# Kernel optimization log

Hardware: AMD Instinct MI355X
Metric: run time of the kernel (lower is better)

Reference implementation:

```python
import jax, jax.numpy as jnp
import numpy as np
import math

C = 256
K = 64
STAGE_NUM = 3
UNFOLD_SIZES = (1, 3, 5)


def _l2norm(t, axis):
    return t / (1e-6 + jnp.linalg.norm(t, axis=axis, keepdims=True))


def setup_inputs() -> dict:
    key = jax.random.key(0)
    k0, k1, k2 = jax.random.split(key, 3)
    b, h, w = 4, 64, 64
    x = jax.random.normal(k0, (b, C, h, w), dtype=jnp.float32)
    mu0 = jax.random.normal(k1, (1, C, K), dtype=jnp.float32) * math.sqrt(2.0 / K)
    mu0 = _l2norm(mu0, axis=1)  # matches buffer init: normal_(0, sqrt(2/k)) then l2norm over c
    w_scalar = jnp.array(1.0, dtype=jnp.float32)
    # convcat: Conv2d(3c, c, 1); init std = sqrt(2 / (1*1*out_channels)) = sqrt(2/c)
    w_cat = jax.random.normal(k2, (C, 3 * C), dtype=jnp.float32) * math.sqrt(2.0 / C)
    b_cat = jnp.zeros((C,), dtype=jnp.float32)
    return {"x": x, "mu0": mu0, "w": w_scalar, "w_cat": w_cat, "b_cat": b_cat}


def _mwi_forward(x, mu0, w, w_cat, b_cat):
    b, c, h, wd = x.shape
    k = mu0.shape[2]
    mu = jnp.broadcast_to(mu0, (b, c, k))
    feats = []
    for s in UNFOLD_SIZES:
        p = (s - 1) // 2
        xp = jnp.pad(x, ((0, 0), (0, 0), (p, p), (p, p)))
        # im2col: (b, c, s*s, h, w), kernel positions row-major -> matches torch F.unfold then view(b,c,-1)
        patches = jnp.stack([xp[:, :, i:i + h, j:j + wd] for i in range(s) for j in range(s)], axis=2)
        ux = patches.reshape(b, c, s * s * h * wd)  # (b, c, N)
        z = None
        for _ in range(STAGE_NUM):  # EM iterations (no_grad in original)
            z = jax.nn.softmax(jnp.einsum('bcn,bck->bnk', ux, mu), axis=2)  # E-step
            z_ = z / (1e-6 + z.sum(axis=1, keepdims=True))
            mu = _l2norm(jnp.einsum('bcn,bnk->bck', ux, z_), axis=1)  # M-step
        mu = jax.lax.stop_gradient(mu)
        z = jax.lax.stop_gradient(z)
        zf = jnp.einsum('bck,bnk->bcn', mu, z)  # reconstruction (b, c, N)
        zf = zf.reshape(b, c, s, s, h, wd)
        # col2im (F.fold): overlap-add of kernel positions
        out = jnp.zeros((b, c, h + 2 * p, wd + 2 * p), dtype=x.dtype)
        for i in range(s):
            for j in range(s):
                out = out.at[:, :, i:i + h, j:j + wd].add(zf[:, :, i, j])
        feats.append(out[:, :, p:p + h, p:p + wd])
    cat = jnp.concatenate(feats, axis=1)  # (b, 3c, h, w)
    u = jnp.einsum('bihw,oi->bohw', cat, w_cat) + b_cat[None, :, None, None]
    out = jax.nn.relu(u * w + x)
    return out, mu


def reference(x, mu0, w, w_cat, b_cat):
    return _mwi_forward(x, mu0, w, w_cat, b_cat)
```

## Files before the change

### kernel.cpp

```cpp
#include <hip/hip_runtime.h>

typedef float f32x4 __attribute__((ext_vector_type(4)));
typedef short bf16x8 __attribute__((ext_vector_type(8)));
typedef unsigned short u16;
typedef u16 u16x8 __attribute__((ext_vector_type(8)));
typedef unsigned int u32;

#define B 4
#define C 256
#define K 64
#define NN 4096
#define W3C 768
#define CP 264
#define SP 72

__device__ __forceinline__ u16 bf_hi(float f) {
    unsigned u = __float_as_uint(f);
    u += 0x7FFFu + ((u >> 16) & 1u);
    return (u16)(u >> 16);
}
__device__ __forceinline__ float bf_f(u16 s) { return __uint_as_float(((unsigned)s) << 16); }

__global__ void k_prep(const float* __restrict__ x, const float* __restrict__ mu0,
                       const float* __restrict__ w_cat,
                       u16* __restrict__ xch, u16* __restrict__ xcl,
                       u16* __restrict__ wch, u16* __restrict__ wcl,
                       u16* __restrict__ muth, u16* __restrict__ mutl) {
    int blk = blockIdx.x, tid = threadIdx.x;
    if (blk < 2048) {
        int i = blk * 256 + tid;
        const float4* s4 = (const float4*)(x + (size_t)i * 8);
        float4 a = s4[0], bq = s4[1];
        float v[8] = {a.x, a.y, a.z, a.w, bq.x, bq.y, bq.z, bq.w};
        u16x8 hv, lv;
        #pragma unroll
        for (int j = 0; j < 8; j++) { u16 hh = bf_hi(v[j]); hv[j] = hh; lv[j] = bf_hi(v[j] - bf_f(hh)); }
        *(u16x8*)(xch + (size_t)i * 8) = hv;
        *(u16x8*)(xcl + (size_t)i * 8) = lv;
    } else if (blk < 2144) {
        int i = (blk - 2048) * 256 + tid;
        const float4* s4 = (const float4*)(w_cat + (size_t)i * 8);
        float4 a = s4[0], bq = s4[1];
        float v[8] = {a.x, a.y, a.z, a.w, bq.x, bq.y, bq.z, bq.w};
        u16x8 hv, lv;
        #pragma unroll
        for (int j = 0; j < 8; j++) { u16 hh = bf_hi(v[j]); hv[j] = hh; lv[j] = bf_hi(v[j] - bf_f(hh)); }
        *(u16x8*)(wch + (size_t)i * 8) = hv;
        *(u16x8*)(wcl + (size_t)i * 8) = lv;
    } else {
        int g = (blk - 2144) * 256 + tid;
        int kq = (g >> 8) & 63, cq = g & 255;
        float v = mu0[cq * K + kq];
        u16 hh = bf_hi(v);
        muth[g] = hh;
        mutl[g] = bf_hi(v - bf_f(hh));
    }
}

__global__ void k_prept(const float* __restrict__ x, u16* __restrict__ th,
                        u16* __restrict__ tl) {
    __shared__ float tile[32][33];
    int b = blockIdx.z, c0 = blockIdx.y * 32, n0 = blockIdx.x * 32;
    int tx = threadIdx.x, ty = threadIdx.y;
    #pragma unroll
    for (int j = 0; j < 4; j++)
        tile[ty + j * 8][tx] = x[((size_t)(b * C + c0 + ty + j * 8)) * NN + n0 + tx];
    __syncthreads();
    #pragma unroll
    for (int j = 0; j < 4; j++) {
        int n = n0 + ty + j * 8;
        float v = tile[tx][ty + j * 8];
        u16 hh = bf_hi(v);
        size_t o = ((size_t)(b * NN + n)) * C + c0 + tx;
        th[o] = hh;
        tl[o] = bf_hi(v - bf_f(hh));
    }
}

__global__ __launch_bounds__(256) void k_em(
        const u16* __restrict__ xth, const u16* __restrict__ xtl,
        const u16* __restrict__ xch, const u16* __restrict__ xcl,
        const u16* __restrict__ muth, const u16* __restrict__ mutl,
        float* __restrict__ tpart, float* __restrict__ dpart,
        u16* __restrict__ sig_out, int pv, int write_sig)
{
    extern __shared__ char smem[];
    u16* smh = (u16*)smem;
    u16* sml = smh + 64 * CP;
    u16* sTh = sml + 64 * CP;
    u16* sTl = sTh + 64 * SP;
    float* redf = (float*)(sTl + 64 * SP);

    const int ch = blockIdx.x, b = blockIdx.y, tid = threadIdx.x;
    const int n0 = ch * 64;

    {
        size_t mbase = ((size_t)(b * K)) * C;
        for (int t = tid; t < 2048; t += 256) {
            int r = t >> 5, cof = (t & 31) * 8;
            *(u16x8*)&smh[r * CP + cof] = *(const u16x8*)&muth[mbase + (size_t)r * C + cof];
            *(u16x8*)&sml[r * CP + cof] = *(const u16x8*)&mutl[mbase + (size_t)r * C + cof];
        }
    }
    __syncthreads();

    const int wid = tid >> 6, l = tid & 63, lg = l >> 4, lr = l & 15;
    f32x4 z4 = {0.f, 0.f, 0.f, 0.f};

    f32x4 acc[4] = {z4, z4, z4, z4};
    {
        const u16* xrh = xth + ((size_t)(b * NN + n0 + wid * 16 + lr)) * C;
        const u16* xrl = xtl + ((size_t)(b * NN + n0 + wid * 16 + lr)) * C;
        for (int cc = 0; cc < 8; cc++) {
            int co = cc * 32 + lg * 8;
            bf16x8 Ah = *(const bf16x8*)&xrh[co];
            bf16x8 Al = *(const bf16x8*)&xrl[co];
            #pragma unroll
            for (int kt = 0; kt < 4; kt++) {
                bf16x8 Bh = *(bf16x8*)&smh[(kt * 16 + lr) * CP + co];
                bf16x8 Bl = *(bf16x8*)&sml[(kt * 16 + lr) * CP + co];
                acc[kt] = __builtin_amdgcn_mfma_f32_16x16x32_bf16(Ah, Bh, acc[kt], 0, 0, 0);
                acc[kt] = __builtin_amdgcn_mfma_f32_16x16x32_bf16(Al, Bh, acc[kt], 0, 0, 0);
                acc[kt] = __builtin_amdgcn_mfma_f32_16x16x32_bf16(Ah, Bl, acc[kt], 0, 0, 0);
            }
        }
    }

    float swv[4][4];
    float psum[4] = {0.f, 0.f, 0.f, 0.f};
    #pragma unroll
    for (int jj = 0; jj < 4; jj++) {
        int n = n0 + wid * 16 + lg * 4 + jj;
        float v0 = acc[0][jj], v1 = acc[1][jj], v2 = acc[2][jj], v3 = acc[3][jj];
        float m = fmaxf(fmaxf(v0, v1), fmaxf(v2, v3));
        #pragma unroll
        for (int off = 1; off <= 8; off <<= 1) m = fmaxf(m, __shfl_xor(m, off));
        float e0 = __expf(v0 - m), e1 = __expf(v1 - m), e2 = __expf(v2 - m), e3 = __expf(v3 - m);
        float ss = e0 + e1 + e2 + e3;
        #pragma unroll
        for (int off = 1; off <= 8; off <<= 1) ss += __shfl_xor(ss, off);
        int y = n >> 6, xx = n & 63;
        float cnt = (float)((min(pv, y) + min(pv, 63 - y) + 1) * (min(pv, xx) + min(pv, 63 - xx) + 1));
        float sc = cnt / ss;
        swv[jj][0] = e0 * sc; swv[jj][1] = e1 * sc; swv[jj][2] = e2 * sc; swv[jj][3] = e3 * sc;
        #pragma unroll
        for (int kt = 0; kt < 4; kt++) {
            psum[kt] += swv[jj][kt];
            if (write_sig)
                sig_out[((size_t)(b * NN + n)) * K + kt * 16 + lr] = bf_hi(swv[jj][kt]);
        }
    }
    #pragma unroll
    for (int kt = 0; kt < 4; kt++) {
        #pragma unroll
        for (int jp = 0; jp < 2; jp++) {
            float va = swv[2 * jp][kt], vb = swv[2 * jp + 1][kt];
            u16 ha = bf_hi(va), hb = bf_hi(vb);
            u16 la = bf_hi(va - bf_f(ha)), lb = bf_hi(vb - bf_f(hb));
            int col = wid * 16 + lg * 4 + 2 * jp;
            *(u32*)&sTh[(kt * 16 + lr) * SP + col] = (u32)ha | ((u32)hb << 16);
            *(u32*)&sTl[(kt * 16 + lr) * SP + col] = (u32)la | ((u32)lb << 16);
        }
        redf[(kt * 16 + lr) * 17 + wid * 4 + lg] = psum[kt];
    }
    __syncthreads();
    if (tid < 64) {
        float sd = 0.f;
        #pragma unroll
        for (int g2 = 0; g2 < 16; g2++) sd += redf[tid * 17 + g2];
        dpart[((size_t)(b * 64 + ch)) * K + tid] = sd;
    }

    f32x4 macc[16];
    #pragma unroll
    for (int ci = 0; ci < 16; ci++) macc[ci] = z4;
    #pragma unroll
    for (int nn2 = 0; nn2 < 2; nn2++) {
        int no = nn2 * 32 + lg * 8;
        bf16x8 Ah = *(bf16x8*)&sTh[(wid * 16 + lr) * SP + no];
        bf16x8 Al = *(bf16x8*)&sTl[(wid * 16 + lr) * SP + no];
        #pragma unroll
        for (int ci = 0; ci < 16; ci++) {
            size_t go = ((size_t)(b * C + ci * 16 + lr)) * NN + n0 + no;
            bf16x8 Bh = *(const bf16x8*)&xch[go];
            bf16x8 Bl = *(const bf16x8*)&xcl[go];
            macc[ci] = __builtin_amdgcn_mfma_f32_16x16x32_bf16(Ah, Bh, macc[ci], 0, 0, 0);
            macc[ci] = __builtin_amdgcn_mfma_f32_16x16x32_bf16(Al, Bh, macc[ci], 0, 0, 0);
            macc[ci] = __builtin_amdgcn_mfma_f32_16x16x32_bf16(Ah, Bl, macc[ci], 0, 0, 0);
        }
    }
    #pragma unroll
    for (int ci = 0; ci < 16; ci++)
        #pragma unroll
        for (int jj = 0; jj < 4; jj++)
            tpart[((size_t)((b * 64 + ch) * K + wid * 16 + lg * 4 + jj)) * C + ci * 16 + lr]
                = macc[ci][jj];
}

__global__ __launch_bounds__(256) void k_norm(
        const float* __restrict__ tpart, const float* __restrict__ dpart,
        u16* __restrict__ muth, u16* __restrict__ mutl,
        float* __restrict__ out_mu, float dconst) {
    __shared__ float red[256];
    __shared__ float dsh;
    int k = blockIdx.x, b = blockIdx.y, tid = threadIdx.x;
    float dv = 0.f;
    if (tid < 64) dv = dpart[((size_t)(b * 64 + tid)) * K + k];
    #pragma unroll
    for (int off = 1; off <= 32; off <<= 1) dv += __shfl_xor(dv, off);
    if (tid == 0) dsh = dv;
    float tt = 0.f;
    #pragma unroll 8
    for (int chn = 0; chn < 64; chn++)
        tt += tpart[((size_t)((b * 64 + chn) * K + k)) * C + tid];
    red[tid] = tt * tt;
    __syncthreads();
    for (int st = 128; st > 0; st >>= 1) {
        if (tid < st) red[tid] += red[tid + st];
        __syncthreads();
    }
    float d = dconst + dsh;
    float inv = 1.f / (1e-6f * d + sqrtf(red[0]));
    float v = tt * inv;
    u16 hh = bf_hi(v);
    size_t o = ((size_t)(b * K + k)) * C + tid;
    muth[o] = hh;
    mutl[o] = bf_hi(v - bf_f(hh));
    out_mu[((size_t)(b * C + tid)) * K + k] = v;
}

__global__ __launch_bounds__(256) void k_pmat(
        const u16* __restrict__ wch, const u16* __restrict__ wcl,
        const u16* __restrict__ mh_g, const u16* __restrict__ ml_g,
        u16* __restrict__ Pb, int s) {
    int ob = blockIdx.x, b = blockIdx.y;
    int tid = threadIdx.x, w = tid >> 6, l = tid & 63, lg = l >> 4, lr = l & 15;
    f32x4 z4 = {0.f, 0.f, 0.f, 0.f};
    f32x4 acc[4] = {z4, z4, z4, z4};
    int orow = ob * 64 + w * 16 + lr;
    const u16* wbh = wch + (size_t)orow * W3C + s * C;
    const u16* wbl = wcl + (size_t)orow * W3C + s * C;
    for (int cc = 0; cc < 8; cc++) {
        int co = cc * 32 + lg * 8;
        bf16x8 Ah = *(const bf16x8*)&wbh[co];
        bf16x8 Al = *(const bf16x8*)&wbl[co];
        #pragma unroll
        for (int kt = 0; kt < 4; kt++) {
            bf16x8 Bh = *(const bf16x8*)&mh_g[((size_t)(b * K + kt * 16 + lr)) * C + co];
            bf16x8 Bl = *(const bf16x8*)&ml_g[((size_t)(b * K + kt * 16 + lr)) * C + co];
            acc[kt] = __builtin_amdgcn_mfma_f32_16x16x32_bf16(Ah, Bh, acc[kt], 0, 0, 0);
            acc[kt] = __builtin_amdgcn_mfma_f32_16x16x32_bf16(Al, Bh, acc[kt], 0, 0, 0);
            acc[kt] = __builtin_amdgcn_mfma_f32_16x16x32_bf16(Ah, Bl, acc[kt], 0, 0, 0);
        }
    }
    #pragma unroll
    for (int kt = 0; kt < 4; kt++)
        #pragma unroll
        for (int jj = 0; jj < 4; jj++) {
            int o = ob * 64 + w * 16 + lg * 4 + jj;
            Pb[((size_t)((s * B + b) * C + o)) * K + kt * 16 + lr] = bf_hi(acc[kt][jj]);
        }
}

__global__ __launch_bounds__(256) void k_final(
        const u16* __restrict__ sh_g, const u16* __restrict__ Pb,
        const float* __restrict__ x, const float* __restrict__ b_cat,
        const float* __restrict__ wscal, float* __restrict__ out) {
    __shared__ u16 ssig[64 * 72];
    __shared__ u16 sP[64 * 72];
    __shared__ float tbuf[64 * 68];
    int nt = blockIdx.x, ot = blockIdx.y, b = blockIdx.z;
    int n0 = nt * 64, o0 = ot * 64;
    int tid = threadIdx.x, w = tid >> 6, l = tid & 63, lg = l >> 4, lr = l & 15;
    f32x4 z4 = {0.f, 0.f, 0.f, 0.f};
    f32x4 acc[4] = {z4, z4, z4, z4};
    for (int s = 0; s < 3; s++) {
        __syncthreads();
        for (int t = tid; t < 512; t += 256) {
            int r = t >> 3, kc = (t & 7) * 8;
            *(u16x8*)&ssig[r * 72 + kc] =
                *(const u16x8*)&sh_g[(size_t)s * ((size_t)B * NN * K) + ((size_t)(b * NN + n0 + r)) * K + kc];
            *(u16x8*)&sP[r * 72 + kc] =
                *(const u16x8*)&Pb[((size_t)((s * B + b) * C + o0 + r)) * K + kc];
        }
        __syncthreads();
        #pragma unroll
        for (int kk = 0; kk < 2; kk++) {
            int ko = kk * 32 + lg * 8;
            bf16x8 A = *(bf16x8*)&ssig[(w * 16 + lr) * 72 + ko];
            #pragma unroll
            for (int oi = 0; oi < 4; oi++) {
                bf16x8 Bv = *(bf16x8*)&sP[(oi * 16 + lr) * 72 + ko];
                acc[oi] = __builtin_amdgcn_mfma_f32_16x16x32_bf16(A, Bv, acc[oi], 0, 0, 0);
            }
        }
    }
    __syncthreads();
    #pragma unroll
    for (int oi = 0; oi < 4; oi++)
        #pragma unroll
        for (int jj = 0; jj < 4; jj++)
            tbuf[(oi * 16 + lr) * 68 + (w * 16 + lg * 4 + jj)] = acc[oi][jj];
    __syncthreads();
    float wv = wscal[0];
    for (int t = tid; t < 1024; t += 256) {
        int ol = t >> 4, ck = (t & 15) * 4;
        int o = o0 + ol;
        float bc = b_cat[o];
        float4 u4 = *(float4*)&tbuf[ol * 68 + ck];
        size_t base = ((size_t)(b * C + o)) * NN + n0 + ck;
        float4 xv = *(const float4*)&x[base];
        float4 r;
        r.x = fmaxf((u4.x + bc) * wv + xv.x, 0.f);
        r.y = fmaxf((u4.y + bc) * wv + xv.y, 0.f);
        r.z = fmaxf((u4.z + bc) * wv + xv.z, 0.f);
        r.w = fmaxf((u4.w + bc) * wv + xv.w, 0.f);
        *(float4*)&out[base] = r;
    }
}

extern "C" void kernel_launch(void* const* d_in, const int* in_sizes, int n_in,
                              void* d_out, int out_size, void* d_ws, size_t ws_size,
                              hipStream_t stream) {
    const float* x     = (const float*)d_in[0];
    const float* mu0   = (const float*)d_in[1];
    const float* wsc   = (const float*)d_in[2];
    const float* w_cat = (const float*)d_in[3];
    const float* b_cat = (const float*)d_in[4];
    float* out = (float*)d_out;
    char* wsb = (char*)d_ws;

    const size_t SZ_X2   = (size_t)B * C * NN * 2;
    const size_t SZ_MUT  = (size_t)B * K * C * 2;
    const size_t SZ_SIGH = (size_t)3 * B * NN * K * 2;
    const size_t SZ_TP   = (size_t)B * 64 * K * C * 4;
    const size_t SZ_DP   = (size_t)B * 64 * K * 4;
    const size_t SZ_PB   = (size_t)3 * B * C * K * 2;
    const size_t SZ_WC   = (size_t)C * W3C * 2;

    size_t off = 0;
    u16*   xch  = (u16*)(wsb + off); off += SZ_X2;
    u16*   xcl  = (u16*)(wsb + off); off += SZ_X2;
    u16*   xth  = (u16*)(wsb + off); off += SZ_X2;
    u16*   xtl  = (u16*)(wsb + off); off += SZ_X2;
    u16*   muth = (u16*)(wsb + off); off += SZ_MUT;
    u16*   mutl = (u16*)(wsb + off); off += SZ_MUT;
    u16*   sigh = (u16*)(wsb + off); off += SZ_SIGH;
    float* tpart= (float*)(wsb + off); off += SZ_TP;
    float* dpart= (float*)(wsb + off); off += SZ_DP;
    u16*   Pb   = (u16*)(wsb + off); off += SZ_PB;
    u16*   wch  = (u16*)(wsb + off); off += SZ_WC;
    u16*   wcl  = (u16*)(wsb + off); off += SZ_WC;
    float* out_mu = out + (size_t)B * C * NN;

    const int EM_LDS = 2 * 64 * CP * 2 + 2 * 64 * SP * 2 + 1088 * 4;
    hipFuncSetAttribute((const void*)k_em, hipFuncAttributeMaxDynamicSharedMemorySize, EM_LDS);

    k_prep<<<2400, 256, 0, stream>>>(x, mu0, w_cat, xch, xcl, wch, wcl, muth, mutl);
    k_prept<<<dim3(128, 8, B), dim3(32, 8), 0, stream>>>(x, xth, xtl);

    const int   pvals[3]   = {0, 1, 2};
    const float dconsts[3] = {1e-6f, 1e-6f + 11.9375f, 1e-6f + 59.4375f};

    for (int s = 0; s < 3; s++) {
        u16* shs = sigh + (size_t)s * ((size_t)B * NN * K);
        for (int it = 0; it < 3; it++) {
            k_em<<<dim3(64, B), 256, EM_LDS, stream>>>(xth, xtl, xch, xcl, muth, mutl,
                                                       tpart, dpart, shs, pvals[s],
                                                       (it == 2) ? 1 : 0);
            k_norm<<<dim3(K, B), 256, 0, stream>>>(tpart, dpart, muth, mutl,
                                                   out_mu, dconsts[s]);
        }
        k_pmat<<<dim3(4, B), 256, 0, stream>>>(wch, wcl, muth, mutl, Pb, s);
    }
    k_final<<<dim3(64, 4, B), 256, 0, stream>>>(sigh, Pb, x, b_cat, wsc, out);
}
```

Before: 298.7 us.

## Fuse EM normalization and projection into EM kernel with atomic accumulation

Removes the separate k_norm and k_pmat launches. The next k_em now normalizes mu from an atomically accumulated per-batch buffer, and the previous scale's projection runs inside k_em on a few blocks. Per-chunk partial tensors are replaced by three rotating buffers filled with atomicAdd, and each k_em zeroes the buffer used by the following iteration. k_em goes to 512 threads, splitting the channel reduction across two wave groups that combine logits through LDS. The cost is heavy atomic contention, redundant normalization work in every block, and floating-point atomic ordering that is not deterministic.

```diff
diff --git a/kernel.cpp b/kernel.cpp
--- a/kernel.cpp
+++ b/kernel.cpp
@@ -13,6 +13,7 @@
 #define W3C 768
 #define CP 264
 #define SP 72
+#define LGP 68
 
 __device__ __forceinline__ u16 bf_hi(float f) {
     unsigned u = __float_as_uint(f);
@@ -25,7 +26,8 @@
                        const float* __restrict__ w_cat,
                        u16* __restrict__ xch, u16* __restrict__ xcl,
                        u16* __restrict__ wch, u16* __restrict__ wcl,
-                       u16* __restrict__ muth, u16* __restrict__ mutl) {
+                       u16* __restrict__ muth, u16* __restrict__ mutl,
+                       float* __restrict__ tp0) {
     int blk = blockIdx.x, tid = threadIdx.x;
     if (blk < 2048) {
         int i = blk * 256 + tid;
@@ -47,13 +49,17 @@
         for (int j = 0; j < 8; j++) { u16 hh = bf_hi(v[j]); hv[j] = hh; lv[j] = bf_hi(v[j] - bf_f(hh)); }
         *(u16x8*)(wch + (size_t)i * 8) = hv;
         *(u16x8*)(wcl + (size_t)i * 8) = lv;
-    } else {
+    } else if (blk < 2400) {
         int g = (blk - 2144) * 256 + tid;
         int kq = (g >> 8) & 63, cq = g & 255;
         float v = mu0[cq * K + kq];
         u16 hh = bf_hi(v);
         muth[g] = hh;
         mutl[g] = bf_hi(v - bf_f(hh));
+    } else {
+        int i = (blk - 2400) * 256 + tid;
+        float4 z = {0.f, 0.f, 0.f, 0.f};
+        *(float4*)&tp0[(size_t)i * 4] = z;
     }
 }
 
@@ -77,180 +83,291 @@
     }
 }
 
-__global__ __launch_bounds__(256) void k_em(
+__global__ __launch_bounds__(512) void k_em(
         const u16* __restrict__ xth, const u16* __restrict__ xtl,
         const u16* __restrict__ xch, const u16* __restrict__ xcl,
         const u16* __restrict__ muth, const u16* __restrict__ mutl,
-        float* __restrict__ tpart, float* __restrict__ dpart,
-        u16* __restrict__ sig_out, int pv, int write_sig)
+        const float* __restrict__ tp_prev, float* __restrict__ tp_cur,
+        float* __restrict__ tp_next, float* __restrict__ dpart,
+        u16* __restrict__ sig_out, u16* __restrict__ Pb,
+        const u16* __restrict__ wch, const u16* __restrict__ wcl,
+        int iter, int pv, float dconst_prev, int write_sig, int s_prev)
+{
+    extern __shared__ char smem[];
+    u16* smh   = (u16*)smem;
+    u16* sml   = smh + 64 * CP;
+    float* slog = (float*)(sml + 64 * CP);
+    u16* sTh   = (u16*)(slog + 64 * LGP);
+    u16* sTl   = sTh + 64 * SP;
+    float* redf = (float*)(sTl + 64 * SP);
+
+    const int ch = blockIdx.x, b = blockIdx.y, tid = threadIdx.x;
+    const int n0 = ch * 64;
+    const int w = tid >> 6, l = tid & 63, lg = l >> 4, lr = l & 15;
+    f32x4 z4 = {0.f, 0.f, 0.f, 0.f};
+
+    if (tid < 256) tp_next[(size_t)b * K * C + ch * 256 + tid] = 0.f;
+
+    float vals[32];
+    float inv = 0.f;
+    int kq = tid >> 3, g = tid & 7;
+    if (iter == 0) {
+        size_t mbase = (size_t)(b * K) * C;
+        for (int t = tid; t < 2048; t += 512) {
+            int r = t >> 5, cof = (t & 31) * 8;
+            *(u16x8*)&smh[r * CP + cof] = *(const u16x8*)&muth[mbase + (size_t)r * C + cof];
+            *(u16x8*)&sml[r * CP + cof] = *(const u16x8*)&mutl[mbase + (size_t)r * C + cof];
+        }
+    } else {
+        if (tid < 64) {
+            float dv = 0.f;
+            #pragma unroll 8
+            for (int c2 = 0; c2 < 64; c2++) dv += dpart[((size_t)(b * 64 + c2)) * K + tid];
+            redf[1088 + tid] = dv;
+        }
+        const float* tp = tp_prev + (size_t)b * K * C + (size_t)kq * C + g * 32;
+        float ssq = 0.f;
+        #pragma unroll
+        for (int j4 = 0; j4 < 8; j4++) {
+            float4 v4 = *(const float4*)&tp[j4 * 4];
+            vals[j4 * 4 + 0] = v4.x; vals[j4 * 4 + 1] = v4.y;
+            vals[j4 * 4 + 2] = v4.z; vals[j4 * 4 + 3] = v4.w;
+            ssq += v4.x * v4.x + v4.y * v4.y + v4.z * v4.z + v4.w * v4.w;
+        }
+        #pragma unroll
+        for (int off = 1; off <= 4; off <<= 1) ssq += __shfl_xor(ssq, off);
+        __syncthreads();
+        float d = dconst_prev + redf[1088 + kq];
+        inv = 1.f / (1e-6f * d + sqrtf(ssq));
+        #pragma unroll
+        for (int j8 = 0; j8 < 4; j8++) {
+            u16x8 hv, lv;
+            #pragma unroll
+            for (int j = 0; j < 8; j++) {
+                float v = vals[j8 * 8 + j] * inv;
+                u16 hh = bf_hi(v);
+                hv[j] = hh; lv[j] = bf_hi(v - bf_f(hh));
+            }
+            *(u16x8*)&smh[kq * CP + g * 32 + j8 * 8] = hv;
+            *(u16x8*)&sml[kq * CP + g * 32 + j8 * 8] = lv;
+        }
+    }
+    __syncthreads();
+
+    if (s_prev >= 0 && ch < 4) {
+        f32x4 pacc[2] = {z4, z4};
+        int orow = ch * 64 + (w & 3) * 16 + lr;
+        const u16* wbh = wch + (size_t)orow * W3C + s_prev * C;
+        const u16* wbl = wcl + (size_t)orow * W3C + s_prev * C;
+        for (int cc = 0; cc < 8; cc++) {
+            int co = cc * 32 + lg * 8;
+            bf16x8 Ah = *(const bf16x8*)&wbh[co];
+            bf16x8 Al = *(const bf16x8*)&wbl[co];
+            #pragma unroll
+            for (int ktl = 0; ktl < 2; ktl++) {
+                int kt = (w >> 2) * 2 + ktl;
+                bf16x8 Bh = *(bf16x8*)&smh[(kt * 16 + lr) * CP + co];
+                bf16x8 Bl = *(bf16x8*)&sml[(kt * 16 + lr) * CP + co];
+                pacc[ktl] = __builtin_amdgcn_mfma_f32_16x16x32_bf16(Ah, Bh, pacc[ktl], 0, 0, 0);
+                pacc[ktl] = __builtin_amdgcn_mfma_f32_16x16x32_bf16(Al, Bh, pacc[ktl], 0, 0, 0);
+                pacc[ktl] = __builtin_amdgcn_mfma_f32_16x16x32_bf16(Ah, Bl, pacc[ktl], 0, 0, 0);
+            }
+        }
+        #pragma unroll
+        for (int ktl = 0; ktl < 2; ktl++)
+            #pragma unroll
+            for (int jj = 0; jj < 4; jj++) {
+                int o = ch * 64 + (w & 3) * 16 + lg * 4 + jj;
+                int kk = ((w >> 2) * 2 + ktl) * 16 + lr;
+                Pb[((size_t)((s_prev * B + b) * C + o)) * K + kk] = bf_hi(pacc[ktl][jj]);
+            }
+    }
+
+    f32x4 acc[4] = {z4, z4, z4, z4};
+    {
+        int chalf = (w >> 2) * 128;
+        const u16* xrh = xth + ((size_t)(b * NN + n0 + (w & 3) * 16 + lr)) * C + chalf;
+        const u16* xrl = xtl + ((size_t)(b * NN + n0 + (w & 3) * 16 + lr)) * C + chalf;
+        for (int cc = 0; cc < 4; cc++) {
+            int co = cc * 32 + lg * 8;
+            bf16x8 Ah = *(const bf16x8*)&xrh[co];
+            bf16x8 Al = *(const bf16x8*)&xrl[co];
+            #pragma unroll
+            for (int kt = 0; kt < 4; kt++) {
+                bf16x8 Bh = *(bf16x8*)&smh[(kt * 16 + lr) * CP + chalf + co];
+                bf16x8 Bl = *(bf16x8*)&sml[(kt * 16 + lr) * CP + chalf + co];
+                acc[kt] = __builtin_amdgcn_mfma_f32_16x16x32_bf16(Ah, Bh, acc[kt], 0, 0, 0);
+                acc[kt] = __builtin_amdgcn_mfma_f32_16x16x32_bf16(Al, Bh, acc[kt], 0, 0, 0);
+                acc[kt] = __builtin_amdgcn_mfma_f32_16x16x32_bf16(Ah, Bl, acc[kt], 0, 0, 0);
+            }
+        }
+    }
+    if (w < 4) {
+        #pragma unroll
+        for (int kt = 0; kt < 4; kt++)
+            #pragma unroll
+            for (int jj = 0; jj < 4; jj++)
+                slog[((w & 3) * 16 + lg * 4 + jj) * LGP + kt * 16 + lr] = acc[kt][jj];
+    }
+    __syncthreads();
+
+    if (w >= 4) {
+        float swv[4][4];
+        float psum[4] = {0.f, 0.f, 0.f, 0.f};
+        #pragma unroll
+        for (int jj = 0; jj < 4; jj++) {
+            int rloc = (w & 3) * 16 + lg * 4 + jj;
+            int n = n0 + rloc;
+            float v0 = acc[0][jj] + slog[rloc * LGP + 0 * 16 + lr];
+            float v1 = acc[1][jj] + slog[rloc * LGP + 1 * 16 + lr];
+            float v2 = acc[2][jj] + slog[rloc * LGP + 2 * 16 + lr];
+            float v3 = acc[3][jj] + slog[rloc * LGP + 3 * 16 + lr];
+            float m = fmaxf(fmaxf(v0, v1), fmaxf(v2, v3));
+            #pragma unroll
+            for (int off = 1; off <= 8; off <<= 1) m = fmaxf(m, __shfl_xor(m, off));
+            float e0 = __expf(v0 - m), e1 = __expf(v1 - m), e2 = __expf(v2 - m), e3 = __expf(v3 - m);
+            float ss = e0 + e1 + e2 + e3;
+            #pragma unroll
+            for (int off = 1; off <= 8; off <<= 1) ss += __shfl_xor(ss, off);
+            int y = n >> 6, xx = n & 63;
+            float cnt = (float)((min(pv, y) + min(pv, 63 - y) + 1) * (min(pv, xx) + min(pv, 63 - xx) + 1));
+            float sc = cnt / ss;
+            swv[jj][0] = e0 * sc; swv[jj][1] = e1 * sc; swv[jj][2] = e2 * sc; swv[jj][3] = e3 * sc;
+            #pragma unroll
+            for (int kt = 0; kt < 4; kt++) {
+                psum[kt] += swv[jj][kt];
+                if (write_sig)
+                    sig_out[((size_t)(b * NN + n)) * K + kt * 16 + lr] = bf_hi(swv[jj][kt]);
+            }
+        }
+        #pragma unroll
+        for (int kt = 0; kt < 4; kt++) {
+            #pragma unroll
+            for (int jp = 0; jp < 2; jp++) {
+                float va = swv[2 * jp][kt], vb = swv[2 * jp + 1][kt];
+                u16 ha = bf_hi(va), hb = bf_hi(vb);
+                u16 la = bf_hi(va - bf_f(ha)), lb = bf_hi(vb - bf_f(hb));
+                int col = (w & 3) * 16 + lg * 4 + 2 * jp;
+                *(u32*)&sTh[(kt * 16 + lr) * SP + col] = (u32)ha | ((u32)hb << 16);
+                *(u32*)&sTl[(kt * 16 + lr) * SP + col] = (u32)la | ((u32)lb << 16);
+            }
+            redf[(kt * 16 + lr) * 17 + (w & 3) * 4 + lg] = psum[kt];
+        }
+    }
+    __syncthreads();
+    if (tid < 64) {
+        float sd = 0.f;
+        #pragma unroll
+        for (int g2 = 0; g2 < 16; g2++) sd += redf[tid * 17 + g2];
+        dpart[((size_t)(b * 64 + ch)) * K + tid] = sd;
+    }
+
+    f32x4 macc[8];
+    #pragma unroll
+    for (int t = 0; t < 8; t++) macc[t] = z4;
+    #pragma unroll
+    for (int nn2 = 0; nn2 < 2; nn2++) {
+        int no = nn2 * 32 + lg * 8;
+        bf16x8 Ah[4], Al[4];
+        #pragma unroll
+        for (int kt2 = 0; kt2 < 4; kt2++) {
+            Ah[kt2] = *(bf16x8*)&sTh[(kt2 * 16 + lr) * SP + no];
+            Al[kt2] = *(bf16x8*)&sTl[(kt2 * 16 + lr) * SP + no];
+        }
+        #pragma unroll
+        for (int cio = 0; cio < 2; cio++) {
+            int c = (w * 2 + cio) * 16 + lr;
+            size_t go = ((size_t)(b * C + c)) * NN + n0 + no;
+            bf16x8 Bh = *(const bf16x8*)&xch[go];
+            bf16x8 Bl = *(const bf16x8*)&xcl[go];
+            #pragma unroll
+            for (int kt2 = 0; kt2 < 4; kt2++) {
+                macc[kt2 * 2 + cio] = __builtin_amdgcn_mfma_f32_16x16x32_bf16(Ah[kt2], Bh, macc[kt2 * 2 + cio], 0, 0, 0);
+                macc[kt2 * 2 + cio] = __builtin_amdgcn_mfma_f32_16x16x32_bf16(Al[kt2], Bh, macc[kt2 * 2 + cio], 0, 0, 0);
+                macc[kt2 * 2 + cio] = __builtin_amdgcn_mfma_f32_16x16x32_bf16(Ah[kt2], Bl, macc[kt2 * 2 + cio], 0, 0, 0);
+            }
+        }
+    }
+    #pragma unroll
+    for (int kt2 = 0; kt2 < 4; kt2++)
+        #pragma unroll
+        for (int cio = 0; cio < 2; cio++)
+            #pragma unroll
+            for (int jj = 0; jj < 4; jj++) {
+                int kk = kt2 * 16 + lg * 4 + jj;
+                int c = (w * 2 + cio) * 16 + lr;
+                atomicAdd(&tp_cur[((size_t)b * K + kk) * C + c], macc[kt2 * 2 + cio][jj]);
+            }
+}
+
+__global__ __launch_bounds__(256) void k_pfinal(
+        const float* __restrict__ tp_last, const float* __restrict__ dpart,
+        const u16* __restrict__ wch, const u16* __restrict__ wcl,
+        u16* __restrict__ Pb, float* __restrict__ out_mu, float dconst)
 {
     extern __shared__ char smem[];
     u16* smh = (u16*)smem;
     u16* sml = smh + 64 * CP;
-    u16* sTh = sml + 64 * CP;
-    u16* sTl = sTh + 64 * SP;
-    float* redf = (float*)(sTl + 64 * SP);
-
-    const int ch = blockIdx.x, b = blockIdx.y, tid = threadIdx.x;
-    const int n0 = ch * 64;
-
+    float* redf = (float*)(sml + 64 * CP);
+    int ob = blockIdx.x, b = blockIdx.y, tid = threadIdx.x;
+    int w = tid >> 6, l = tid & 63, lg = l >> 4, lr = l & 15;
+    if (tid < 64) {
+        float dv = 0.f;
+        #pragma unroll 8
+        for (int c2 = 0; c2 < 64; c2++) dv += dpart[((size_t)(b * 64 + c2)) * K + tid];
+        redf[tid] = dv;
+    }
+    __syncthreads();
     {
-        size_t mbase = ((size_t)(b * K)) * C;
-        for (int t = tid; t < 2048; t += 256) {
-            int r = t >> 5, cof = (t & 31) * 8;
-            *(u16x8*)&smh[r * CP + cof] = *(const u16x8*)&muth[mbase + (size_t)r * C + cof];
-            *(u16x8*)&sml[r * CP + cof] = *(const u16x8*)&mutl[mbase + (size_t)r * C + cof];
-        }
-    }
-    __syncthreads();
-
-    const int wid = tid >> 6, l = tid & 63, lg = l >> 4, lr = l & 15;
-    f32x4 z4 = {0.f, 0.f, 0.f, 0.f};
-
-    f32x4 acc[4] = {z4, z4, z4, z4};
-    {
-        const u16* xrh = xth + ((size_t)(b * NN + n0 + wid * 16 + lr)) * C;
-        const u16* xrl = xtl + ((size_t)(b * NN + n0 + wid * 16 + lr)) * C;
-        for (int cc = 0; cc < 8; cc++) {
-            int co = cc * 32 + lg * 8;
-            bf16x8 Ah = *(const bf16x8*)&xrh[co];
-            bf16x8 Al = *(const bf16x8*)&xrl[co];
-            #pragma unroll
-            for (int kt = 0; kt < 4; kt++) {
-                bf16x8 Bh = *(bf16x8*)&smh[(kt * 16 + lr) * CP + co];
-                bf16x8 Bl = *(bf16x8*)&sml[(kt * 16 + lr) * CP + co];
-                acc[kt] = __builtin_amdgcn_mfma_f32_16x16x32_bf16(Ah, Bh, acc[kt], 0, 0, 0);
-                acc[kt] = __builtin_amdgcn_mfma_f32_16x16x32_bf16(Al, Bh, acc[kt], 0, 0, 0);
-                acc[kt] = __builtin_amdgcn_mfma_f32_16x16x32_bf16(Ah, Bl, acc[kt], 0, 0, 0);
-            }
-        }
-    }
-
-    float swv[4][4];
-    float psum[4] = {0.f, 0.f, 0.f, 0.f};
-    #pragma unroll
-    for (int jj = 0; jj < 4; jj++) {
-        int n = n0 + wid * 16 + lg * 4 + jj;
-        float v0 = acc[0][jj], v1 = acc[1][jj], v2 = acc[2][jj], v3 = acc[3][jj];
-        float m = fmaxf(fmaxf(v0, v1), fmaxf(v2, v3));
-        #pragma unroll
-        for (int off = 1; off <= 8; off <<= 1) m = fmaxf(m, __shfl_xor(m, off));
-        float e0 = __expf(v0 - m), e1 = __expf(v1 - m), e2 = __expf(v2 - m), e3 = __expf(v3 - m);
-        float ss = e0 + e1 + e2 + e3;
-        #pragma unroll
-        for (int off = 1; off <= 8; off <<= 1) ss += __shfl_xor(ss, off);
-        int y = n >> 6, xx = n & 63;
-        float cnt = (float)((min(pv, y) + min(pv, 63 - y) + 1) * (min(pv, xx) + min(pv, 63 - xx) + 1));
-        float sc = cnt / ss;
-        swv[jj][0] = e0 * sc; swv[jj][1] = e1 * sc; swv[jj][2] = e2 * sc; swv[jj][3] = e3 * sc;
-        #pragma unroll
-        for (int kt = 0; kt < 4; kt++) {
-            psum[kt] += swv[jj][kt];
-            if (write_sig)
-                sig_out[((size_t)(b * NN + n)) * K + kt * 16 + lr] = bf_hi(swv[jj][kt]);
-        }
-    }
-    #pragma unroll
-    for (int kt = 0; kt < 4; kt++) {
-        #pragma unroll
-        for (int jp = 0; jp < 2; jp++) {
-            float va = swv[2 * jp][kt], vb = swv[2 * jp + 1][kt];
-            u16 ha = bf_hi(va), hb = bf_hi(vb);
-            u16 la = bf_hi(va - bf_f(ha)), lb = bf_hi(vb - bf_f(hb));
-            int col = wid * 16 + lg * 4 + 2 * jp;
-            *(u32*)&sTh[(kt * 16 + lr) * SP + col] = (u32)ha | ((u32)hb << 16);
-            *(u32*)&sTl[(kt * 16 + lr) * SP + col] = (u32)la | ((u32)lb << 16);
-        }
-        redf[(kt * 16 + lr) * 17 + wid * 4 + lg] = psum[kt];
-    }
-    __syncthreads();
-    if (tid < 64) {
-        float sd = 0.f;
-        #pragma unroll
-        for (int g2 = 0; g2 < 16; g2++) sd += redf[tid * 17 + g2];
-        dpart[((size_t)(b * 64 + ch)) * K + tid] = sd;
-    }
-
-    f32x4 macc[16];
-    #pragma unroll
-    for (int ci = 0; ci < 16; ci++) macc[ci] = z4;
-    #pragma unroll
-    for (int nn2 = 0; nn2 < 2; nn2++) {
-        int no = nn2 * 32 + lg * 8;
-        bf16x8 Ah = *(bf16x8*)&sTh[(wid * 16 + lr) * SP + no];
-        bf16x8 Al = *(bf16x8*)&sTl[(wid * 16 + lr) * SP + no];
-        #pragma unroll
-        for (int ci = 0; ci < 16; ci++) {
-            size_t go = ((size_t)(b * C + ci * 16 + lr)) * NN + n0 + no;
-            bf16x8 Bh = *(const bf16x8*)&xch[go];
-            bf16x8 Bl = *(const bf16x8*)&xcl[go];
-            macc[ci] = __builtin_amdgcn_mfma_f32_16x16x32_bf16(Ah, Bh, macc[ci], 0, 0, 0);
-            macc[ci] = __builtin_amdgcn_mfma_f32_16x16x32_bf16(Al, Bh, macc[ci], 0, 0, 0);
-            macc[ci] = __builtin_amdgcn_mfma_f32_16x16x32_bf16(Ah, Bl, macc[ci], 0, 0, 0);
-        }
-    }
-    #pragma unroll
-    for (int ci = 0; ci < 16; ci++)
-        #pragma unroll
-        for (int jj = 0; jj < 4; jj++)
-            tpart[((size_t)((b * 64 + ch) * K + wid * 16 + lg * 4 + jj)) * C + ci * 16 + lr]
-                = macc[ci][jj];
-}
-
-__global__ __launch_bounds__(256) void k_norm(
-        const float* __restrict__ tpart, const float* __restrict__ dpart,
-        u16* __restrict__ muth, u16* __restrict__ mutl,
-        float* __restrict__ out_mu, float dconst) {
-    __shared__ float red[256];
-    __shared__ float dsh;
-    int k = blockIdx.x, b = blockIdx.y, tid = threadIdx.x;
-    float dv = 0.f;
-    if (tid < 64) dv = dpart[((size_t)(b * 64 + tid)) * K + k];
-    #pragma unroll
-    for (int off = 1; off <= 32; off <<= 1) dv += __shfl_xor(dv, off);
-    if (tid == 0) dsh = dv;
-    float tt = 0.f;
-    #pragma unroll 8
-    for (int chn = 0; chn < 64; chn++)
-        tt += tpart[((size_t)((b * 64 + chn) * K + k)) * C + tid];
-    red[tid] = tt * tt;
-    __syncthreads();
-    for (int st = 128; st > 0; st >>= 1) {
-        if (tid < st) red[tid] += red[tid + st];
-        __syncthreads();
-    }
-    float d = dconst + dsh;
-    float inv = 1.f / (1e-6f * d + sqrtf(red[0]));
-    float v = tt * inv;
-    u16 hh = bf_hi(v);
-    size_t o = ((size_t)(b * K + k)) * C + tid;
-    muth[o] = hh;
-    mutl[o] = bf_hi(v - bf_f(hh));
-    out_mu[((size_t)(b * C + tid)) * K + k] = v;
-}
-
-__global__ __launch_bounds__(256) void k_pmat(
-        const u16* __restrict__ wch, const u16* __restrict__ wcl,
-        const u16* __restrict__ mh_g, const u16* __restrict__ ml_g,
-        u16* __restrict__ Pb, int s) {
-    int ob = blockIdx.x, b = blockIdx.y;
-    int tid = threadIdx.x, w = tid >> 6, l = tid & 63, lg = l >> 4, lr = l & 15;
-    f32x4 z4 = {0.f, 0.f, 0.f, 0.f};
-    f32x4 acc[4] = {z4, z4, z4, z4};
+        int kq = tid >> 2, g = tid & 3;
+        const float* tp = tp_last + (size_t)b * K * C + (size_t)kq * C + g * 64;
+        float vals[64];
+        float ssq = 0.f;
+        #pragma unroll
+        for (int j4 = 0; j4 < 16; j4++) {
+            float4 v4 = *(const float4*)&tp[j4 * 4];
+            vals[j4 * 4 + 0] = v4.x; vals[j4 * 4 + 1] = v4.y;
+            vals[j4 * 4 + 2] = v4.z; vals[j4 * 4 + 3] = v4.w;
+            ssq += v4.x * v4.x + v4.y * v4.y + v4.z * v4.z + v4.w * v4.w;
+        }
+        ssq += __shfl_xor(ssq, 1);
+        ssq += __shfl_xor(ssq, 2);
+        float d = dconst + redf[kq];
+        float inv = 1.f / (1e-6f * d + sqrtf(ssq));
+        #pragma unroll
+        for (int j8 = 0; j8 < 8; j8++) {
+            u16x8 hv, lv;
+            #pragma unroll
+            for (int j = 0; j < 8; j++) {
+                float v = vals[j8 * 8 + j] * inv;
+                u16 hh = bf_hi(v);
+                hv[j] = hh; lv[j] = bf_hi(v - bf_f(hh));
+            }
+            *(u16x8*)&smh[kq * CP + g * 64 + j8 * 8] = hv;
+            *(u16x8*)&sml[kq * CP + g * 64 + j8 * 8] = lv;
+        }
+        if (ob == 0) {
+            #pragma unroll 8
+            for (int j = 0; j < 64; j++)
+                out_mu[((size_t)(b * C + g * 64 + j)) * K + kq] = vals[j] * inv;
+        }
+    }
+    __syncthreads();
+    f32x4 pacc[4] = {{0.f,0.f,0.f,0.f},{0.f,0.f,0.f,0.f},{0.f,0.f,0.f,0.f},{0.f,0.f,0.f,0.f}};
     int orow = ob * 64 + w * 16 + lr;
-    const u16* wbh = wch + (size_t)orow * W3C + s * C;
-    const u16* wbl = wcl + (size_t)orow * W3C + s * C;
+    const u16* wbh = wch + (size_t)orow * W3C + 2 * C;
+    const u16* wbl = wcl + (size_t)orow * W3C + 2 * C;
     for (int cc = 0; cc < 8; cc++) {
         int co = cc * 32 + lg * 8;
         bf16x8 Ah = *(const bf16x8*)&wbh[co];
         bf16x8 Al = *(const bf16x8*)&wbl[co];
         #pragma unroll
         for (int kt = 0; kt < 4; kt++) {
-            bf16x8 Bh = *(const bf16x8*)&mh_g[((size_t)(b * K + kt * 16 + lr)) * C + co];
-            bf16x8 Bl = *(const bf16x8*)&ml_g[((size_t)(b * K + kt * 16 + lr)) * C + co];
-            acc[kt] = __builtin_amdgcn_mfma_f32_16x16x32_bf16(Ah, Bh, acc[kt], 0, 0, 0);
-            acc[kt] = __builtin_amdgcn_mfma_f32_16x16x32_bf16(Al, Bh, acc[kt], 0, 0, 0);
-            acc[kt] = __builtin_amdgcn_mfma_f32_16x16x32_bf16(Ah, Bl, acc[kt], 0, 0, 0);
+            bf16x8 Bh = *(bf16x8*)&smh[(kt * 16 + lr) * CP + co];
+            bf16x8 Bl = *(bf16x8*)&sml[(kt * 16 + lr) * CP + co];
+            pacc[kt] = __builtin_amdgcn_mfma_f32_16x16x32_bf16(Ah, Bh, pacc[kt], 0, 0, 0);
+            pacc[kt] = __builtin_amdgcn_mfma_f32_16x16x32_bf16(Al, Bh, pacc[kt], 0, 0, 0);
+            pacc[kt] = __builtin_amdgcn_mfma_f32_16x16x32_bf16(Ah, Bl, pacc[kt], 0, 0, 0);
         }
     }
     #pragma unroll
@@ -258,7 +375,7 @@
         #pragma unroll
         for (int jj = 0; jj < 4; jj++) {
             int o = ob * 64 + w * 16 + lg * 4 + jj;
-            Pb[((size_t)((s * B + b) * C + o)) * K + kt * 16 + lr] = bf_hi(acc[kt][jj]);
+            Pb[((size_t)((2 * B + b) * C + o)) * K + kt * 16 + lr] = bf_hi(pacc[kt][jj]);
         }
 }
 
@@ -333,7 +450,7 @@
     const size_t SZ_X2   = (size_t)B * C * NN * 2;
     const size_t SZ_MUT  = (size_t)B * K * C * 2;
     const size_t SZ_SIGH = (size_t)3 * B * NN * K * 2;
-    const size_t SZ_TP   = (size_t)B * 64 * K * C * 4;
+    const size_t SZ_TPB  = (size_t)B * K * C * 4;
     const size_t SZ_DP   = (size_t)B * 64 * K * 4;
     const size_t SZ_PB   = (size_t)3 * B * C * K * 2;
     const size_t SZ_WC   = (size_t)C * W3C * 2;
@@ -346,32 +463,39 @@
     u16*   muth = (u16*)(wsb + off); off += SZ_MUT;
     u16*   mutl = (u16*)(wsb + off); off += SZ_MUT;
     u16*   sigh = (u16*)(wsb + off); off += SZ_SIGH;
-    float* tpart= (float*)(wsb + off); off += SZ_TP;
+    float* tpb0 = (float*)(wsb + off); off += SZ_TPB;
+    float* tpb1 = (float*)(wsb + off); off += SZ_TPB;
+    float* tpb2 = (float*)(wsb + off); off += SZ_TPB;
     float* dpart= (float*)(wsb + off); off += SZ_DP;
     u16*   Pb   = (u16*)(wsb + off); off += SZ_PB;
     u16*   wch  = (u16*)(wsb + off); off += SZ_WC;
     u16*   wcl  = (u16*)(wsb + off); off += SZ_WC;
     float* out_mu = out + (size_t)B * C * NN;
-
-    const int EM_LDS = 2 * 64 * CP * 2 + 2 * 64 * SP * 2 + 1088 * 4;
+    float* bufs[3] = {tpb0, tpb1, tpb2};
+
+    const int EM_LDS = 2 * 64 * CP * 2 + 64 * LGP * 4 + 2 * 64 * SP * 2 + 1152 * 4;
+    const int PF_LDS = 2 * 64 * CP * 2 + 64 * 4;
     hipFuncSetAttribute((const void*)k_em, hipFuncAttributeMaxDynamicSharedMemorySize, EM_LDS);
-
-    k_prep<<<2400, 256, 0, stream>>>(x, mu0, w_cat, xch, xcl, wch, wcl, muth, mutl);
+    hipFuncSetAttribute((const void*)k_pfinal, hipFuncAttributeMaxDynamicSharedMemorySize, PF_LDS);
+
+    k_prep<<<2464, 256, 0, stream>>>(x, mu0, w_cat, xch, xcl, wch, wcl, muth, mutl, tpb0);
     k_prept<<<dim3(128, 8, B), dim3(32, 8), 0, stream>>>(x, xth, xtl);
 
     const int   pvals[3]   = {0, 1, 2};
     const float dconsts[3] = {1e-6f, 1e-6f + 11.9375f, 1e-6f + 59.4375f};
 
-    for (int s = 0; s < 3; s++) {
+    for (int i = 0; i < 9; i++) {
+        int s = i / 3;
         u16* shs = sigh + (size_t)s * ((size_t)B * NN * K);
-        for (int it = 0; it < 3; it++) {
-            k_em<<<dim3(64, B), 256, EM_LDS, stream>>>(xth, xtl, xch, xcl, muth, mutl,
-                                                       tpart, dpart, shs, pvals[s],
-                                                       (it == 2) ? 1 : 0);
-            k_norm<<<dim3(K, B), 256, 0, stream>>>(tpart, dpart, muth, mutl,
-                                                   out_mu, dconsts[s]);
-        }
-        k_pmat<<<dim3(4, B), 256, 0, stream>>>(wch, wcl, muth, mutl, Pb, s);
-    }
+        float dprev = (i > 0) ? dconsts[(i - 1) / 3] : 0.f;
+        int s_prev = (i > 0 && i % 3 == 0) ? (i / 3 - 1) : -1;
+        k_em<<<dim3(64, B), 512, EM_LDS, stream>>>(
+            xth, xtl, xch, xcl, muth, mutl,
+            bufs[(i + 2) % 3], bufs[i % 3], bufs[(i + 1) % 3], dpart,
+            shs, Pb, wch, wcl,
+            i, pvals[s], dprev, (i % 3 == 2) ? 1 : 0, s_prev);
+    }
+    k_pfinal<<<dim3(4, B), 256, PF_LDS, stream>>>(bufs[8 % 3], dpart, wch, wcl,
+                                                  Pb, out_mu, dconsts[2]);
     k_final<<<dim3(64, 4, B), 256, 0, stream>>>(sigh, Pb, x, b_cat, wsc, out);
 }
```

Result: faster. 290.7 us (-2.7%).
